# Optimization experiments

Measured on AMD Instinct MI355X. Metric: run time of the kernel, lower is better.

Reference implementation:

```python
import jax, jax.numpy as jnp
import numpy as np

EMBED_DIM = 1024
NUM_HEADS = 16
HEAD_DIM = EMBED_DIM // NUM_HEADS  # 64
QK_SCALE = 0.125  # head_dim ** -0.5, passed as qk_scale in __init__
B, LQ, LKV = 2, 2048, 2048


def setup_inputs() -> dict:
    key = jax.random.key(0)
    ks = jax.random.split(key, 7)
    std = 0.02
    return {
        "q": jax.random.normal(ks[0], (B, LQ, EMBED_DIM), dtype=jnp.float32),
        "k": jax.random.normal(ks[1], (B, LKV, EMBED_DIM), dtype=jnp.float32),
        "v": jax.random.normal(ks[2], (B, LKV, EMBED_DIM), dtype=jnp.float32),
        "Wq": jax.random.normal(ks[3], (EMBED_DIM, EMBED_DIM), dtype=jnp.float32) * std,
        "Wk": jax.random.normal(ks[4], (EMBED_DIM, EMBED_DIM), dtype=jnp.float32) * std,
        "Wv": jax.random.normal(ks[5], (EMBED_DIM, EMBED_DIM), dtype=jnp.float32) * std,
        "Wo": jax.random.normal(ks[6], (EMBED_DIM, EMBED_DIM), dtype=jnp.float32) * std,
    }


def _split_heads(x):
    # rearrange 'b l (c n) -> b n l c' with n = num_heads (heads are the INNER sub-dim)
    b, l, _ = x.shape
    return x.reshape(b, l, HEAD_DIM, NUM_HEADS).transpose(0, 3, 1, 2)  # (b, n, l, c)


def reference(q, k, v, Wq, Wk, Wv, Wo):
    b = q.shape[0]
    qh = _split_heads(q @ Wq)  # (b, n, lq, c)
    kh = _split_heads(k @ Wk)  # (b, n, lkv, c)
    vh = _split_heads(v @ Wv)  # (b, n, lkv, c)
    # attn = (q * qk_scale) @ k^T / sqrt(batch)
    scores = jnp.einsum('bnqc,bnkc->bnqk', qh * QK_SCALE, kh)
    scores = scores / jnp.sqrt(jnp.float32(b))
    attn = jax.nn.softmax(scores, axis=-1)
    out = jnp.einsum('bnqk,bnkc->bnqc', attn, vh)  # (b, n, lq, c)
    # merge heads back with the inverse of the (c n) split: b n l c -> b l (c n)
    out = out.transpose(0, 2, 3, 1).reshape(b, -1, HEAD_DIM * NUM_HEADS)
    return out @ Wo  # output projection (b, lq, embed_dim)
```

## Files before the change

### kernel.cpp

```cpp
#include <hip/hip_runtime.h>
#include <hip/hip_bf16.h>


typedef __attribute__((ext_vector_type(8))) short short8;
typedef __attribute__((ext_vector_type(4))) float f32x4;
typedef __attribute__((ext_vector_type(16))) float f32x16;
typedef __hip_bfloat16 bf16;

#define GLD16(g, l) __builtin_amdgcn_global_load_lds( \
    (const __attribute__((address_space(1))) void*)(g), \
    (__attribute__((address_space(3))) void*)(l), 16, 0, 0)

__device__ __forceinline__ f32x4 mfma16(short8 a, short8 b, f32x4 c) {
  return __builtin_amdgcn_mfma_f32_16x16x32_bf16(a, b, c, 0, 0, 0);
}
__device__ __forceinline__ f32x16 mfma32(short8 a, short8 b, f32x16 c) {
  return __builtin_amdgcn_mfma_f32_32x32x16_bf16(a, b, c, 0, 0, 0);
}

union B8 { bf16 h[8]; int4 v; };
union B4 { bf16 h[4]; int2 v; };

#define QK_SCALE_TOT 0.08838834764831845f
#define SC2f (QK_SCALE_TOT * 1.4426950408889634f)

__device__ __forceinline__ float fexp2(float x) {
#if __has_builtin(__builtin_amdgcn_exp2f)
  return __builtin_amdgcn_exp2f(x);
#else
  return exp2f(x);
#endif
}

__device__ __forceinline__ int cvtpk(float lo, float hi_) {
  int r;
  asm("v_cvt_pk_bf16_f32 %0, %1, %2" : "=v"(r) : "v"(lo), "v"(hi_));
  return r;
}

#define ZV16 {0.f,0.f,0.f,0.f,0.f,0.f,0.f,0.f,0.f,0.f,0.f,0.f,0.f,0.f,0.f,0.f}

__global__ __launch_bounds__(256) void cast3_kernel(
    const float* __restrict__ q, const float* __restrict__ k,
    const float* __restrict__ v, bf16* __restrict__ out)
{
  const float* src = (blockIdx.y == 0) ? q : (blockIdx.y == 1) ? k : v;
  bf16* dst = out + (size_t)blockIdx.y * (4u << 20);
  size_t i = ((size_t)blockIdx.x * 256 + threadIdx.x) * 8;
  float4 a = *(const float4*)(src + i);
  float4 b = *(const float4*)(src + i + 4);
  B8 u;
  u.h[0] = __float2bfloat16(a.x); u.h[1] = __float2bfloat16(a.y);
  u.h[2] = __float2bfloat16(a.z); u.h[3] = __float2bfloat16(a.w);
  u.h[4] = __float2bfloat16(b.x); u.h[5] = __float2bfloat16(b.y);
  u.h[6] = __float2bfloat16(b.z); u.h[7] = __float2bfloat16(b.w);
  *(int4*)(dst + i) = u.v;
}

__global__ __launch_bounds__(256) void wtrans_kernel(
    const float* __restrict__ Wq, const float* __restrict__ Wk,
    const float* __restrict__ Wv, const float* __restrict__ Wo,
    bf16* __restrict__ dstbase)
{
  __shared__ bf16 ld[64][68];
  const int z = blockIdx.z;
  const float* src = (z == 0) ? Wq : (z == 1) ? Wk : (z == 2) ? Wv : Wo;
  bf16* dst = dstbase + (size_t)z * (1u << 20);
  const int k0 = blockIdx.x * 64, n0 = blockIdx.y * 64;
  const int t = threadIdx.x;
  const bool perm = (z == 3);
#pragma unroll
  for (int it = 0; it < 4; ++it) {
    int kk = it * 16 + (t >> 4);
    int K = k0 + kk;
    int j = perm ? ((K & 63) * 16 + (K >> 6)) : K;
    float4 vv = *(const float4*)(src + (size_t)j * 1024 + n0 + (t & 15) * 4);
    int c = (t & 15) * 4;
    ld[c + 0][kk] = __float2bfloat16(vv.x);
    ld[c + 1][kk] = __float2bfloat16(vv.y);
    ld[c + 2][kk] = __float2bfloat16(vv.z);
    ld[c + 3][kk] = __float2bfloat16(vv.w);
  }
  __syncthreads();
#pragma unroll
  for (int it = 0; it < 2; ++it) {
    int rr = it * 32 + (t >> 3), cc = (t & 7) * 8;
    B8 u;
#pragma unroll
    for (int e = 0; e < 8; ++e) u.h[e] = ld[rr][cc + e];
    *(int4*)(dst + (size_t)(n0 + rr) * 1024 + k0 + cc) = u.v;
  }
}

template<int FINAL>
__global__ __launch_bounds__(256) void gemm_kernel(
    const bf16* __restrict__ Abase, const bf16* __restrict__ WTbase,
    bf16* __restrict__ Qh, bf16* __restrict__ Kh, bf16* __restrict__ VhT,
    float* __restrict__ Cout)
{
  __shared__ bf16 lA[128 * 64];
  __shared__ bf16 lB[128 * 64];
  const int t = threadIdx.x, lane = t & 63;
  const int wv = t >> 6, wr = wv >> 1, wc = wv & 1;
  const int l15 = lane & 15, yi8 = (lane >> 4) * 8;
  const int tN = blockIdx.x * 128, tM = blockIdx.y * 128;
  const int z = FINAL ? 0 : blockIdx.z;

  const bf16* A  = Abase  + (size_t)z * (4u << 20);
  const bf16* BT = WTbase + (size_t)z * (1u << 20);

  const int sr = t >> 3, sc8 = (t & 7) * 8;
  size_t aoff[4], boff[4];
#pragma unroll
  for (int i = 0; i < 4; ++i) {
    int row = tM + i * 32 + sr;
    if (FINAL) {
      aoff[i] = (size_t)(row >> 11) * 16 * (2048 * 64) + (size_t)(row & 2047) * 64 + sc8;
    } else {
      aoff[i] = (size_t)row * 1024 + sc8;
    }
    boff[i] = (size_t)(tN + i * 32 + sr) * 1024 + sc8;
  }
  const size_t astep = FINAL ? (size_t)(2048 * 64) : 64;

  f32x4 acc[4][4];
#pragma unroll
  for (int m = 0; m < 4; ++m)
#pragma unroll
    for (int n = 0; n < 4; ++n) acc[m][n] = {0.f, 0.f, 0.f, 0.f};

  for (int kt = 0; kt < 16; ++kt) {
#pragma unroll
    for (int i = 0; i < 4; ++i) GLD16(A + aoff[i], &lA[i * 2048 + t * 8]);
#pragma unroll
    for (int i = 0; i < 4; ++i) GLD16(BT + boff[i], &lB[i * 2048 + t * 8]);
#pragma unroll
    for (int i = 0; i < 4; ++i) { aoff[i] += astep; boff[i] += 64; }
    __syncthreads();
#pragma unroll
    for (int kk = 0; kk < 2; ++kk) {
      short8 af[4], bfr[4];
#pragma unroll
      for (int m = 0; m < 4; ++m)
        af[m] = *(const short8*)&lA[(wr * 64 + m * 16 + l15) * 64 + kk * 32 + yi8];
#pragma unroll
      for (int n = 0; n < 4; ++n)
        bfr[n] = *(const short8*)&lB[(wc * 64 + n * 16 + l15) * 64 + kk * 32 + yi8];
#pragma unroll
      for (int m = 0; m < 4; ++m)
#pragma unroll
        for (int n = 0; n < 4; ++n)
          acc[m][n] = mfma16(af[m], bfr[n], acc[m][n]);
    }
    __syncthreads();
  }

#pragma unroll
  for (int m = 0; m < 4; ++m) {
#pragma unroll
    for (int n = 0; n < 4; ++n) {
      int col = tN + wc * 64 + n * 16 + l15;
      int rbase = tM + wr * 64 + m * 16 + (lane >> 4) * 4;
      if (FINAL) {
#pragma unroll
        for (int j = 0; j < 4; ++j)
          Cout[(size_t)(rbase + j) * 1024 + col] = acc[m][n][j];
      } else if (z == 2) {
        int nh = col & 15, c = col >> 4;
        int b = rbase >> 11, l0 = rbase & 2047;
        B4 u;
#pragma unroll
        for (int j = 0; j < 4; ++j) u.h[j] = __float2bfloat16(acc[m][n][j]);
        *(int2*)&VhT[((size_t)(b * 16 + nh) * 64 + c) * 2048 + l0] = u.v;
      } else {
        bf16* dst = z ? Kh : Qh;
        int nh = col & 15, c = col >> 4;
#pragma unroll
        for (int j = 0; j < 4; ++j) {
          int row = rbase + j;
          dst[((size_t)((row >> 11) * 16 + nh) * 2048 + (row & 2047)) * 64 + c] =
              __float2bfloat16(acc[m][n][j]);
        }
      }
    }
  }
}

__global__ __launch_bounds__(256) void attn_kernel(
    const bf16* __restrict__ Qh, const bf16* __restrict__ Kh,
    const bf16* __restrict__ VhT, bf16* __restrict__ Oh)
{
  __shared__ bf16 Kt[2][64 * 64];
  __shared__ bf16 Vt[2][64 * 64];
  const int t = threadIdx.x, lane = t & 63, w = t >> 6;
  const int l31 = lane & 31, hi = lane >> 5;
  const int bh = blockIdx.y;
  const int q0 = blockIdx.x * 128 + w * 32;
  const size_t baseQK = (size_t)bh * (2048 * 64);
  const size_t baseV  = (size_t)bh * (64 * 2048);

  short8 qf[4];
#pragma unroll
  for (int kc = 0; kc < 4; ++kc)
    qf[kc] = *(const short8*)&Qh[baseQK + (size_t)(q0 + l31) * 64 + kc * 16 + hi * 8];

  const int r0 = t >> 3, g0 = t & 7;
  const int sg = (g0 ^ (r0 & 7)) * 8;
  const bf16* ksrc0 = Kh  + baseQK + (size_t)r0 * 64 + sg;
  const bf16* ksrc1 = Kh  + baseQK + (size_t)(r0 + 32) * 64 + sg;
  const bf16* vsrc0 = VhT + baseV  + (size_t)r0 * 2048 + sg;
  const bf16* vsrc1 = VhT + baseV  + (size_t)(r0 + 32) * 2048 + sg;

  auto stage = [&](int buf, int ti) {
    GLD16(ksrc0 + (size_t)ti * 4096, &Kt[buf][t * 8]);
    GLD16(ksrc1 + (size_t)ti * 4096, &Kt[buf][2048 + t * 8]);
    GLD16(vsrc0 + ti * 64,           &Vt[buf][t * 8]);
    GLD16(vsrc1 + ti * 64,           &Vt[buf][2048 + t * 8]);
  };

  f32x16 o0 = ZV16, o1 = ZV16;
  float m = -1e30f, l = 0.f;
  const int swz = (l31 & 7);

  stage(0, 0);
  for (int ti = 0; ti < 32; ++ti) {
    const int buf = ti & 1;
    __syncthreads();
    if (ti < 31) stage(buf ^ 1, ti + 1);

    f32x16 s0 = ZV16, s1 = ZV16;
    __builtin_amdgcn_s_setprio(1);
#pragma unroll
    for (int kc = 0; kc < 4; ++kc) {
      const int gr = ((kc * 2 + hi) ^ swz) * 8;
      short8 kf0 = *(const short8*)&Kt[buf][l31 * 64 + gr];
      short8 kf1 = *(const short8*)&Kt[buf][(32 + l31) * 64 + gr];
      s0 = mfma32(kf0, qf[kc], s0);
      s1 = mfma32(kf1, qf[kc], s1);
    }
    __builtin_amdgcn_s_setprio(0);

    float tm8[8];
#pragma unroll
    for (int i2 = 0; i2 < 8; ++i2)
      tm8[i2] = fmaxf(fmaxf(s0[i2], s0[i2 + 8]), fmaxf(s1[i2], s1[i2 + 8]));
    float pm = fmaxf(fmaxf(fmaxf(tm8[0], tm8[1]), fmaxf(tm8[2], tm8[3])),
                     fmaxf(fmaxf(tm8[4], tm8[5]), fmaxf(tm8[6], tm8[7])));
    pm = fmaxf(pm, __shfl_xor(pm, 32));
    float mn = fmaxf(m, pm);
    float corr = fexp2((m - mn) * SC2f);
    m = mn;
    float nb = -mn * SC2f;
#pragma unroll
    for (int r = 0; r < 16; ++r) {
      s0[r] = fexp2(s0[r] * SC2f + nb);
      s1[r] = fexp2(s1[r] * SC2f + nb);
    }
    float ts8[8];
#pragma unroll
    for (int i2 = 0; i2 < 8; ++i2)
      ts8[i2] = (s0[i2] + s0[i2 + 8]) + (s1[i2] + s1[i2 + 8]);
    float rs = ((ts8[0] + ts8[1]) + (ts8[2] + ts8[3])) +
               ((ts8[4] + ts8[5]) + (ts8[6] + ts8[7]));
    rs += __shfl_xor(rs, 32);
    l = l * corr + rs;
#pragma unroll
    for (int r = 0; r < 16; ++r) { o0[r] *= corr; o1[r] *= corr; }

    short8 pf[4];
    {
      union U { int i[4]; short8 s8; } fr[4];
      int wds[16];
#pragma unroll
      for (int j = 0; j < 8; ++j) wds[j]     = cvtpk(s0[2 * j], s0[2 * j + 1]);
#pragma unroll
      for (int j = 0; j < 8; ++j) wds[8 + j] = cvtpk(s1[2 * j], s1[2 * j + 1]);
#pragma unroll
      for (int fb = 0; fb < 4; ++fb) {
        int a0 = wds[fb * 4 + 0], a1 = wds[fb * 4 + 1];
        int a2 = wds[fb * 4 + 2], a3 = wds[fb * 4 + 3];
#if __has_builtin(__builtin_amdgcn_permlane32_swap)
        auto s02 = __builtin_amdgcn_permlane32_swap(a0, a2, false, false);
        auto s13 = __builtin_amdgcn_permlane32_swap(a1, a3, false, false);
        fr[fb].i[0] = s02[0]; fr[fb].i[1] = s13[0];
        fr[fb].i[2] = s02[1]; fr[fb].i[3] = s13[1];
#else
        int x0 = __shfl_xor(a0, 32), x2 = __shfl_xor(a2, 32);
        int x1 = __shfl_xor(a1, 32), x3 = __shfl_xor(a3, 32);
        fr[fb].i[0] = hi ? x2 : a0; fr[fb].i[1] = hi ? x3 : a1;
        fr[fb].i[2] = hi ? a2 : x0; fr[fb].i[3] = hi ? a3 : x1;
#endif
        pf[fb] = fr[fb].s8;
      }
    }

    __builtin_amdgcn_s_setprio(1);
#pragma unroll
    for (int kc = 0; kc < 4; ++kc) {
      const int gr = ((kc * 2 + hi) ^ swz) * 8;
      short8 vf0 = *(const short8*)&Vt[buf][l31 * 64 + gr];
      short8 vf1 = *(const short8*)&Vt[buf][(32 + l31) * 64 + gr];
      o0 = mfma32(vf0, pf[kc], o0);
      o1 = mfma32(vf1, pf[kc], o1);
    }
    __builtin_amdgcn_s_setprio(0);
  }

  float rl = 1.0f / l;
  bf16* orow = Oh + baseQK + (size_t)(q0 + l31) * 64;
#pragma unroll
  for (int rq = 0; rq < 4; ++rq) {
    B4 u0, u1;
#pragma unroll
    for (int j = 0; j < 4; ++j) {
      u0.h[j] = __float2bfloat16(o0[rq * 4 + j] * rl);
      u1.h[j] = __float2bfloat16(o1[rq * 4 + j] * rl);
    }
    int dbase = rq * 8 + hi * 4;
    *(int2*)&orow[dbase]      = u0.v;
    *(int2*)&orow[32 + dbase] = u1.v;
  }
}

extern "C" void kernel_launch(void* const* d_in, const int* in_sizes, int n_in,
                              void* d_out, int out_size, void* d_ws, size_t ws_size,
                              hipStream_t stream) {
  const float* q  = (const float*)d_in[0];
  const float* k  = (const float*)d_in[1];
  const float* v  = (const float*)d_in[2];
  const float* Wq = (const float*)d_in[3];
  const float* Wk = (const float*)d_in[4];
  const float* Wv = (const float*)d_in[5];
  const float* Wo = (const float*)d_in[6];
  char* ws = (char*)d_ws;
  const size_t MB = 1u << 20;
  bf16* xb  = (bf16*)(ws);
  bf16* WT  = (bf16*)(ws + 24 * MB);
  bf16* Qh  = (bf16*)(ws + 32 * MB);
  bf16* Kh  = (bf16*)(ws + 40 * MB);
  bf16* VhT = (bf16*)(ws + 48 * MB);
  bf16* Oh  = (bf16*)(ws);

  cast3_kernel<<<dim3(2048, 3), 256, 0, stream>>>(q, k, v, xb);
  wtrans_kernel<<<dim3(16, 16, 4), 256, 0, stream>>>(Wq, Wk, Wv, Wo, WT);
  gemm_kernel<0><<<dim3(8, 32, 3), 256, 0, stream>>>(xb, WT, Qh, Kh, VhT, nullptr);
  attn_kernel<<<dim3(16, 32), 256, 0, stream>>>(Qh, Kh, VhT, Oh);
  gemm_kernel<1><<<dim3(8, 32), 256, 0, stream>>>(Oh, WT + 3 * (1u << 20), Qh, Kh, VhT,
                                                  (float*)d_out);
}
```

Measured before the change: 284.6 us.

## Rewrite projection GEMMs as 256x256 tile, 8-wave double-buffered pipelined kernel

```diff
diff --git a/kernel.cpp b/kernel.cpp
--- a/kernel.cpp
+++ b/kernel.cpp
@@ -10,6 +10,11 @@
 #define GLD16(g, l) __builtin_amdgcn_global_load_lds( \
     (const __attribute__((address_space(1))) void*)(g), \
     (__attribute__((address_space(3))) void*)(l), 16, 0, 0)
+
+#define VMCNT(n) do { asm volatile("s_waitcnt vmcnt(" #n ")" ::: "memory"); \
+                      __builtin_amdgcn_sched_barrier(0); } while (0)
+#define BAR() do { __builtin_amdgcn_sched_barrier(0); __builtin_amdgcn_s_barrier(); \
+                   __builtin_amdgcn_sched_barrier(0); } while (0)
 
 __device__ __forceinline__ f32x4 mfma16(short8 a, short8 b, f32x4 c) {
   return __builtin_amdgcn_mfma_f32_16x16x32_bf16(a, b, c, 0, 0, 0);
@@ -93,74 +98,149 @@
 }
 
 template<int FINAL>
-__global__ __launch_bounds__(256) void gemm_kernel(
+__global__ __launch_bounds__(512, 2) void gemm8_kernel(
     const bf16* __restrict__ Abase, const bf16* __restrict__ WTbase,
     bf16* __restrict__ Qh, bf16* __restrict__ Kh, bf16* __restrict__ VhT,
     float* __restrict__ Cout)
 {
-  __shared__ bf16 lA[128 * 64];
-  __shared__ bf16 lB[128 * 64];
-  const int t = threadIdx.x, lane = t & 63;
-  const int wv = t >> 6, wr = wv >> 1, wc = wv & 1;
-  const int l15 = lane & 15, yi8 = (lane >> 4) * 8;
-  const int tN = blockIdx.x * 128, tM = blockIdx.y * 128;
+  __shared__ bf16 lA[2][2][128 * 64];
+  __shared__ bf16 lB[2][2][128 * 64];
+  const int t = threadIdx.x, lane = t & 63, w = t >> 6;
+  const int wr = w >> 2, wc = w & 3;
+  const int l15 = lane & 15, l16 = lane >> 4;
+  const int rswE = ((l15 >> 2) & 1) << 4;
+  const int tN = blockIdx.x * 256, tM = blockIdx.y * 256;
   const int z = FINAL ? 0 : blockIdx.z;
-
   const bf16* A  = Abase  + (size_t)z * (4u << 20);
   const bf16* BT = WTbase + (size_t)z * (1u << 20);
 
-  const int sr = t >> 3, sc8 = (t & 7) * 8;
-  size_t aoff[4], boff[4];
-#pragma unroll
-  for (int i = 0; i < 4; ++i) {
-    int row = tM + i * 32 + sr;
-    if (FINAL) {
-      aoff[i] = (size_t)(row >> 11) * 16 * (2048 * 64) + (size_t)(row & 2047) * 64 + sc8;
-    } else {
-      aoff[i] = (size_t)row * 1024 + sc8;
-    }
-    boff[i] = (size_t)(tN + i * 32 + sr) * 1024 + sc8;
-  }
-  const size_t astep = FINAL ? (size_t)(2048 * 64) : 64;
-
-  f32x4 acc[4][4];
-#pragma unroll
-  for (int m = 0; m < 4; ++m)
+  int oj[2], srj[2], scj[2];
+#pragma unroll
+  for (int j = 0; j < 2; ++j) {
+    int o = (w * 2 + j) * 1024 + lane * 16;
+    int lg = o ^ (((o >> 9) & 1) << 5);
+    oj[j] = o >> 1;
+    srj[j] = lg >> 7;
+    scj[j] = (lg & 127) >> 1;
+  }
+  size_t aRow[2][2], bRow[2][2];
+#pragma unroll
+  for (int h = 0; h < 2; ++h)
+#pragma unroll
+    for (int j = 0; j < 2; ++j) {
+      int r = tM + h * 128 + srj[j];
+      if (FINAL)
+        aRow[h][j] = ((size_t)(r >> 11) * 16 * 2048 + (r & 2047)) * 64 + scj[j];
+      else
+        aRow[h][j] = (size_t)r * 1024 + scj[j];
+      bRow[h][j] = (size_t)(tN + h * 128 + srj[j]) * 1024 + scj[j];
+    }
+  const size_t aK = FINAL ? (size_t)(2048 * 64) : 64;
+
+  auto stageA_ = [&](int buf, int h, int kt) {
+    GLD16(A + aRow[h][0] + (size_t)kt * aK, &lA[buf][h][oj[0]]);
+    GLD16(A + aRow[h][1] + (size_t)kt * aK, &lA[buf][h][oj[1]]);
+  };
+  auto stageB_ = [&](int buf, int h, int kt) {
+    GLD16(BT + bRow[h][0] + (size_t)kt * 64, &lB[buf][h][oj[0]]);
+    GLD16(BT + bRow[h][1] + (size_t)kt * 64, &lB[buf][h][oj[1]]);
+  };
+  auto readA = [&](int buf, int m, int kk) -> short8 {
+    return *(const short8*)&lA[buf][wr]
+        [(m * 16 + l15) * 64 + ((kk * 32 + l16 * 8) ^ rswE)];
+  };
+  auto readB = [&](int buf, int n, int kk) -> short8 {
+    return *(const short8*)&lB[buf][wc >> 1]
+        [((wc & 1) * 64 + n * 16 + l15) * 64 + ((kk * 32 + l16 * 8) ^ rswE)];
+  };
+
+  f32x4 acc[8][4];
+#pragma unroll
+  for (int m = 0; m < 8; ++m)
 #pragma unroll
     for (int n = 0; n < 4; ++n) acc[m][n] = {0.f, 0.f, 0.f, 0.f};
 
-  for (int kt = 0; kt < 16; ++kt) {
-#pragma unroll
-    for (int i = 0; i < 4; ++i) GLD16(A + aoff[i], &lA[i * 2048 + t * 8]);
-#pragma unroll
-    for (int i = 0; i < 4; ++i) GLD16(BT + boff[i], &lB[i * 2048 + t * 8]);
-#pragma unroll
-    for (int i = 0; i < 4; ++i) { aoff[i] += astep; boff[i] += 64; }
-    __syncthreads();
-#pragma unroll
-    for (int kk = 0; kk < 2; ++kk) {
-      short8 af[4], bfr[4];
-#pragma unroll
-      for (int m = 0; m < 4; ++m)
-        af[m] = *(const short8*)&lA[(wr * 64 + m * 16 + l15) * 64 + kk * 32 + yi8];
-#pragma unroll
-      for (int n = 0; n < 4; ++n)
-        bfr[n] = *(const short8*)&lB[(wc * 64 + n * 16 + l15) * 64 + kk * 32 + yi8];
-#pragma unroll
-      for (int m = 0; m < 4; ++m)
+  stageB_(0, 0, 0); stageB_(0, 1, 0);
+  stageA_(0, 0, 0); stageA_(0, 1, 0);
+  stageB_(1, 0, 1); stageB_(1, 1, 1);
+  VMCNT(4);
+  BAR();
+
+  const int NIT = 8;
+  for (int i = 0; i < NIT; ++i) {
+    const bool more = (i + 1 < NIT);
+    const int k0 = 2 * i;
+    short8 bfr[4][2];
+#pragma unroll
+    for (int q = 0; q < 4; ++q) {
+      if (q == 0) {
 #pragma unroll
         for (int n = 0; n < 4; ++n)
-          acc[m][n] = mfma16(af[m], bfr[n], acc[m][n]);
-    }
-    __syncthreads();
-  }
-
-#pragma unroll
-  for (int m = 0; m < 4; ++m) {
+#pragma unroll
+          for (int kk = 0; kk < 2; ++kk) bfr[n][kk] = readB(0, n, kk);
+      }
+      short8 af[2][2];
+#pragma unroll
+      for (int mm = 0; mm < 2; ++mm)
+#pragma unroll
+        for (int kk = 0; kk < 2; ++kk) af[mm][kk] = readA(0, 2 * q + mm, kk);
+      if (q == 0) stageA_(1, 0, k0 + 1);
+      else if (q == 1) stageA_(1, 1, k0 + 1);
+      else if (q == 2) { if (more) stageB_(0, 0, k0 + 2); }
+      else             { if (more) stageB_(0, 1, k0 + 2); }
+      BAR();
+      __builtin_amdgcn_s_setprio(1);
+#pragma unroll
+      for (int mm = 0; mm < 2; ++mm)
+#pragma unroll
+        for (int n = 0; n < 4; ++n)
+#pragma unroll
+          for (int kk = 0; kk < 2; ++kk)
+            acc[2 * q + mm][n] = mfma16(af[mm][kk], bfr[n][kk], acc[2 * q + mm][n]);
+      __builtin_amdgcn_s_setprio(0);
+      if (q == 3) { if (more) { VMCNT(4); } else { VMCNT(0); } }
+      BAR();
+    }
+#pragma unroll
+    for (int q = 0; q < 4; ++q) {
+      if (q == 0) {
+#pragma unroll
+        for (int n = 0; n < 4; ++n)
+#pragma unroll
+          for (int kk = 0; kk < 2; ++kk) bfr[n][kk] = readB(1, n, kk);
+      }
+      short8 af[2][2];
+#pragma unroll
+      for (int mm = 0; mm < 2; ++mm)
+#pragma unroll
+        for (int kk = 0; kk < 2; ++kk) af[mm][kk] = readA(1, 2 * q + mm, kk);
+      if (more) {
+        if (q == 0) stageA_(0, 0, k0 + 2);
+        else if (q == 1) stageA_(0, 1, k0 + 2);
+        else if (q == 2) stageB_(1, 0, k0 + 3);
+        else stageB_(1, 1, k0 + 3);
+      }
+      BAR();
+      __builtin_amdgcn_s_setprio(1);
+#pragma unroll
+      for (int mm = 0; mm < 2; ++mm)
+#pragma unroll
+        for (int n = 0; n < 4; ++n)
+#pragma unroll
+          for (int kk = 0; kk < 2; ++kk)
+            acc[2 * q + mm][n] = mfma16(af[mm][kk], bfr[n][kk], acc[2 * q + mm][n]);
+      __builtin_amdgcn_s_setprio(0);
+      if (q == 3 && more) VMCNT(4);
+      BAR();
+    }
+  }
+
+#pragma unroll
+  for (int m = 0; m < 8; ++m) {
 #pragma unroll
     for (int n = 0; n < 4; ++n) {
       int col = tN + wc * 64 + n * 16 + l15;
-      int rbase = tM + wr * 64 + m * 16 + (lane >> 4) * 4;
+      int rbase = tM + wr * 128 + m * 16 + l16 * 4;
       if (FINAL) {
 #pragma unroll
         for (int j = 0; j < 4; ++j)
@@ -343,8 +423,8 @@
 
   cast3_kernel<<<dim3(2048, 3), 256, 0, stream>>>(q, k, v, xb);
   wtrans_kernel<<<dim3(16, 16, 4), 256, 0, stream>>>(Wq, Wk, Wv, Wo, WT);
-  gemm_kernel<0><<<dim3(8, 32, 3), 256, 0, stream>>>(xb, WT, Qh, Kh, VhT, nullptr);
+  gemm8_kernel<0><<<dim3(4, 16, 3), 512, 0, stream>>>(xb, WT, Qh, Kh, VhT, nullptr);
   attn_kernel<<<dim3(16, 32), 256, 0, stream>>>(Qh, Kh, VhT, Oh);
-  gemm_kernel<1><<<dim3(8, 32), 256, 0, stream>>>(Oh, WT + 3 * (1u << 20), Qh, Kh, VhT,
-                                                  (float*)d_out);
-}
+  gemm8_kernel<1><<<dim3(4, 16), 512, 0, stream>>>(Oh, WT + 3 * (1u << 20), Qh, Kh, VhT,
+                                                   (float*)d_out);
+}
```

Result: slower. 300.9 us (+5.7%).

## Double-buffer GEMM LDS tiles with swizzle, larger QKV tiles and block remap

Applied to the files above, without the earlier changes.

```diff
diff --git a/kernel.cpp b/kernel.cpp
--- a/kernel.cpp
+++ b/kernel.cpp
@@ -92,80 +92,86 @@
   }
 }
 
-template<int FINAL>
-__global__ __launch_bounds__(256) void gemm_kernel(
+__global__ __launch_bounds__(512, 2) void gemm2p_kernel(
     const bf16* __restrict__ Abase, const bf16* __restrict__ WTbase,
-    bf16* __restrict__ Qh, bf16* __restrict__ Kh, bf16* __restrict__ VhT,
-    float* __restrict__ Cout)
+    bf16* __restrict__ Qh, bf16* __restrict__ Kh, bf16* __restrict__ VhT)
 {
-  __shared__ bf16 lA[128 * 64];
-  __shared__ bf16 lB[128 * 64];
-  const int t = threadIdx.x, lane = t & 63;
-  const int wv = t >> 6, wr = wv >> 1, wc = wv & 1;
-  const int l15 = lane & 15, yi8 = (lane >> 4) * 8;
-  const int tN = blockIdx.x * 128, tM = blockIdx.y * 128;
-  const int z = FINAL ? 0 : blockIdx.z;
-
+  __shared__ bf16 lA[2][256 * 64];
+  __shared__ bf16 lB[2][256 * 64];
+  const int t = threadIdx.x, lane = t & 63, w = t >> 6;
+  const int wr = w >> 2, wc = w & 3;
+  const int l15 = lane & 15, l16 = lane >> 4;
+  const int rswE = ((l15 >> 2) & 1) << 4;
+  const int nblk = blockIdx.x + 4 * blockIdx.y;
+  const int sblk = (nblk & 7) * 8 + (nblk >> 3);
+  const int tN = (sblk & 3) * 256, tM = (sblk >> 2) * 256;
+  const int z = blockIdx.z;
   const bf16* A  = Abase  + (size_t)z * (4u << 20);
   const bf16* BT = WTbase + (size_t)z * (1u << 20);
 
-  const int sr = t >> 3, sc8 = (t & 7) * 8;
-  size_t aoff[4], boff[4];
+  int oo[4];
+  size_t aRow[4], bRow[4];
 #pragma unroll
   for (int i = 0; i < 4; ++i) {
-    int row = tM + i * 32 + sr;
-    if (FINAL) {
-      aoff[i] = (size_t)(row >> 11) * 16 * (2048 * 64) + (size_t)(row & 2047) * 64 + sc8;
-    } else {
-      aoff[i] = (size_t)row * 1024 + sc8;
-    }
-    boff[i] = (size_t)(tN + i * 32 + sr) * 1024 + sc8;
-  }
-  const size_t astep = FINAL ? (size_t)(2048 * 64) : 64;
-
-  f32x4 acc[4][4];
-#pragma unroll
-  for (int m = 0; m < 4; ++m)
+    int o = i * 8192 + t * 16;
+    int lg = o ^ (((o >> 9) & 1) << 5);
+    oo[i] = o >> 1;
+    int sr = lg >> 7;
+    int sc = (lg & 127) >> 1;
+    aRow[i] = (size_t)(tM + sr) * 1024 + sc;
+    bRow[i] = (size_t)(tN + sr) * 1024 + sc;
+  }
+
+  auto stage = [&](int buf, int kt) {
+#pragma unroll
+    for (int i = 0; i < 4; ++i)
+      GLD16(A + aRow[i] + (size_t)kt * 64, &lA[buf][oo[i]]);
+#pragma unroll
+    for (int i = 0; i < 4; ++i)
+      GLD16(BT + bRow[i] + (size_t)kt * 64, &lB[buf][oo[i]]);
+  };
+
+  f32x4 acc[8][4];
+#pragma unroll
+  for (int m = 0; m < 8; ++m)
 #pragma unroll
     for (int n = 0; n < 4; ++n) acc[m][n] = {0.f, 0.f, 0.f, 0.f};
 
+  stage(0, 0);
+  __syncthreads();
+
   for (int kt = 0; kt < 16; ++kt) {
-#pragma unroll
-    for (int i = 0; i < 4; ++i) GLD16(A + aoff[i], &lA[i * 2048 + t * 8]);
-#pragma unroll
-    for (int i = 0; i < 4; ++i) GLD16(BT + boff[i], &lB[i * 2048 + t * 8]);
-#pragma unroll
-    for (int i = 0; i < 4; ++i) { aoff[i] += astep; boff[i] += 64; }
-    __syncthreads();
+    const int cur = kt & 1;
+    if (kt < 15) stage(cur ^ 1, kt + 1);
 #pragma unroll
     for (int kk = 0; kk < 2; ++kk) {
-      short8 af[4], bfr[4];
-#pragma unroll
-      for (int m = 0; m < 4; ++m)
-        af[m] = *(const short8*)&lA[(wr * 64 + m * 16 + l15) * 64 + kk * 32 + yi8];
+      short8 bfr[4], af[8];
 #pragma unroll
       for (int n = 0; n < 4; ++n)
-        bfr[n] = *(const short8*)&lB[(wc * 64 + n * 16 + l15) * 64 + kk * 32 + yi8];
-#pragma unroll
-      for (int m = 0; m < 4; ++m)
+        bfr[n] = *(const short8*)&lB[cur]
+            [(wc * 64 + n * 16 + l15) * 64 + ((kk * 32 + l16 * 8) ^ rswE)];
+#pragma unroll
+      for (int m = 0; m < 8; ++m)
+        af[m] = *(const short8*)&lA[cur]
+            [(wr * 128 + m * 16 + l15) * 64 + ((kk * 32 + l16 * 8) ^ rswE)];
+      __builtin_amdgcn_s_setprio(1);
+#pragma unroll
+      for (int m = 0; m < 8; ++m)
 #pragma unroll
         for (int n = 0; n < 4; ++n)
           acc[m][n] = mfma16(af[m], bfr[n], acc[m][n]);
+      __builtin_amdgcn_s_setprio(0);
     }
     __syncthreads();
   }
 
 #pragma unroll
-  for (int m = 0; m < 4; ++m) {
+  for (int m = 0; m < 8; ++m) {
 #pragma unroll
     for (int n = 0; n < 4; ++n) {
       int col = tN + wc * 64 + n * 16 + l15;
-      int rbase = tM + wr * 64 + m * 16 + (lane >> 4) * 4;
-      if (FINAL) {
-#pragma unroll
-        for (int j = 0; j < 4; ++j)
-          Cout[(size_t)(rbase + j) * 1024 + col] = acc[m][n][j];
-      } else if (z == 2) {
+      int rbase = tM + wr * 128 + m * 16 + l16 * 4;
+      if (z == 2) {
         int nh = col & 15, c = col >> 4;
         int b = rbase >> 11, l0 = rbase & 2047;
         B4 u;
@@ -184,6 +190,89 @@
       }
     }
   }
+}
+
+__global__ __launch_bounds__(256) void gemmo_kernel(
+    const bf16* __restrict__ Oh, const bf16* __restrict__ WoT,
+    float* __restrict__ Cout)
+{
+  __shared__ bf16 lA[2][128 * 64];
+  __shared__ bf16 lB[2][128 * 64];
+  const int t = threadIdx.x, lane = t & 63, w = t >> 6;
+  const int wr = w >> 1, wc = w & 1;
+  const int l15 = lane & 15, l16 = lane >> 4;
+  const int rswE = ((l15 >> 2) & 1) << 4;
+  const int nblk = blockIdx.x + 8 * blockIdx.y;
+  const int sblk = (nblk & 7) * 32 + (nblk >> 3);
+  const int tN = (sblk & 7) * 128, tM = (sblk >> 3) * 128;
+
+  int oo[4];
+  size_t aRow[4], bRow[4];
+#pragma unroll
+  for (int i = 0; i < 4; ++i) {
+    int o = i * 4096 + t * 16;
+    int lg = o ^ (((o >> 9) & 1) << 5);
+    oo[i] = o >> 1;
+    int sr = lg >> 7;
+    int sc = (lg & 127) >> 1;
+    int rg = tM + sr;
+    aRow[i] = ((size_t)(rg >> 11) * 16 * 2048 + (rg & 2047)) * 64 + sc;
+    bRow[i] = (size_t)(tN + sr) * 1024 + sc;
+  }
+
+  auto stage = [&](int buf, int kt) {
+#pragma unroll
+    for (int i = 0; i < 4; ++i)
+      GLD16(Oh + aRow[i] + (size_t)kt * (2048 * 64), &lA[buf][oo[i]]);
+#pragma unroll
+    for (int i = 0; i < 4; ++i)
+      GLD16(WoT + bRow[i] + kt * 64, &lB[buf][oo[i]]);
+  };
+
+  f32x4 acc[4][4];
+#pragma unroll
+  for (int m = 0; m < 4; ++m)
+#pragma unroll
+    for (int n = 0; n < 4; ++n) acc[m][n] = {0.f, 0.f, 0.f, 0.f};
+
+  stage(0, 0);
+  __syncthreads();
+
+  for (int kt = 0; kt < 16; ++kt) {
+    const int cur = kt & 1;
+    if (kt < 15) stage(cur ^ 1, kt + 1);
+#pragma unroll
+    for (int kk = 0; kk < 2; ++kk) {
+      short8 bfr[4], af[4];
+#pragma unroll
+      for (int n = 0; n < 4; ++n)
+        bfr[n] = *(const short8*)&lB[cur]
+            [(wc * 64 + n * 16 + l15) * 64 + ((kk * 32 + l16 * 8) ^ rswE)];
+#pragma unroll
+      for (int m = 0; m < 4; ++m)
+        af[m] = *(const short8*)&lA[cur]
+            [(wr * 64 + m * 16 + l15) * 64 + ((kk * 32 + l16 * 8) ^ rswE)];
+      __builtin_amdgcn_s_setprio(1);
+#pragma unroll
+      for (int m = 0; m < 4; ++m)
+#pragma unroll
+        for (int n = 0; n < 4; ++n)
+          acc[m][n] = mfma16(af[m], bfr[n], acc[m][n]);
+      __builtin_amdgcn_s_setprio(0);
+    }
+    __syncthreads();
+  }
+
+#pragma unroll
+  for (int m = 0; m < 4; ++m)
+#pragma unroll
+    for (int n = 0; n < 4; ++n) {
+      int col = tN + wc * 64 + n * 16 + l15;
+      int rbase = tM + wr * 64 + m * 16 + l16 * 4;
+#pragma unroll
+      for (int j = 0; j < 4; ++j)
+        Cout[(size_t)(rbase + j) * 1024 + col] = acc[m][n][j];
+    }
 }
 
 __global__ __launch_bounds__(256) void attn_kernel(
@@ -343,8 +432,8 @@
 
   cast3_kernel<<<dim3(2048, 3), 256, 0, stream>>>(q, k, v, xb);
   wtrans_kernel<<<dim3(16, 16, 4), 256, 0, stream>>>(Wq, Wk, Wv, Wo, WT);
-  gemm_kernel<0><<<dim3(8, 32, 3), 256, 0, stream>>>(xb, WT, Qh, Kh, VhT, nullptr);
+  gemm2p_kernel<<<dim3(4, 16, 3), 512, 0, stream>>>(xb, WT, Qh, Kh, VhT);
   attn_kernel<<<dim3(16, 32), 256, 0, stream>>>(Qh, Kh, VhT, Oh);
-  gemm_kernel<1><<<dim3(8, 32), 256, 0, stream>>>(Oh, WT + 3 * (1u << 20), Qh, Kh, VhT,
-                                                  (float*)d_out);
-}
+  gemmo_kernel<<<dim3(8, 32), 256, 0, stream>>>(Oh, WT + 3 * (1u << 20),
+                                                (float*)d_out);
+}
```

Result: faster. 277.3 us (-2.6%).
